# Optimization experiments

Measured on AMD Instinct MI355X. Metric: run time of the kernel, lower is better.

The kernel has to match this reference:

```python
import jax, jax.numpy as jnp
import numpy as np

N_EDGES, N_CH = 4, 2
N_NODES = 8192
IN_C, OUT_C = 64, 64


def setup_inputs() -> dict:
    key = jax.random.key(0)
    k1, k2, k3, k4, k5 = jax.random.split(key, 5)
    A = jax.random.uniform(k1, (N_EDGES, N_NODES, N_NODES), dtype=jnp.float32)
    X = jax.random.normal(k2, (N_NODES, IN_C), dtype=jnp.float32)
    weight = jax.random.normal(k3, (N_EDGES, N_CH), dtype=jnp.float32)
    # torch Linear: weight [out, in], bias [out]
    lin_w = jax.random.normal(k4, (OUT_C, IN_C), dtype=jnp.float32) / np.sqrt(IN_C)
    lin_b = jax.random.normal(k5, (OUT_C,), dtype=jnp.float32) * 0.01
    bias = jnp.zeros((OUT_C,), dtype=jnp.float32)
    return {"A": A, "X": X, "weight": weight, "lin_w": lin_w, "lin_b": lin_b, "bias": bias}


def reference(A, X, weight, lin_w, lin_b, bias):
    # softmax over edge dim (dim=0), then the double loop collapses to a
    # per-edge scale: A_agg = sum_i (sum_j fw[i,j]) * A[i]
    fw = jax.nn.softmax(weight, axis=0)          # [E, C]
    scale = fw.sum(axis=1)                        # [E]
    A_agg = jnp.einsum('e,enm->nm', scale, A)     # [N, N]
    H = A_agg @ X                                 # [N, in_c]
    H = H @ lin_w.T + lin_b + bias                # [N, out_c]
    return H
```

## Files before the change

### kernel.cpp

```cpp
#include <hip/hip_runtime.h>
#include <math.h>


#define NN 8192
#define CH 64
#define RB 16
#define KT 64
#define NT (NN / KT)
#define NBLK (NN / RB)

#define A_BUF_F 4096
#define OFF_A0 0
#define OFF_A1 (A_BUF_F)
#define OFF_X0 (2 * A_BUF_F)
#define AGG_STRIDE_S 72
#define AGG_F ((RB * AGG_STRIDE_S) / 2)
#define HT_STRIDE 68
#define XPACK_UINTS_PER_TILE 2048

typedef __attribute__((ext_vector_type(8))) short bf16x8;
typedef __attribute__((ext_vector_type(4))) float f32x4;

__device__ __forceinline__ void dma16(const float* g, float* l) {
  __builtin_amdgcn_global_load_lds(
      (const __attribute__((address_space(1))) void*)g,
      (__attribute__((address_space(3))) void*)l, 16, 0, 0);
}

__device__ __forceinline__ unsigned f2bfu(float f) {
  unsigned u = __float_as_uint(f);
  return (u + 0x7FFFu + ((u >> 16) & 1u)) >> 16;
}

__global__ __launch_bounds__(256)
void gtn_packX(const float* __restrict__ X, unsigned* __restrict__ ws) {
  const int F = blockIdx.x * 256 + threadIdx.x;
  const int t = F >> 9, rem = F & 511;
  const int wv = rem >> 7, kt = (rem >> 6) & 1, lane = rem & 63;
  const int fm = lane & 15, fg = lane >> 4;
  const int c = wv * 16 + fm;
  const int bk = t * KT + kt * 32 + fg * 8;
  uint4 o;
  o.x = f2bfu(X[(size_t)(bk + 0) * CH + c]) | (f2bfu(X[(size_t)(bk + 1) * CH + c]) << 16);
  o.y = f2bfu(X[(size_t)(bk + 2) * CH + c]) | (f2bfu(X[(size_t)(bk + 3) * CH + c]) << 16);
  o.z = f2bfu(X[(size_t)(bk + 4) * CH + c]) | (f2bfu(X[(size_t)(bk + 5) * CH + c]) << 16);
  o.w = f2bfu(X[(size_t)(bk + 6) * CH + c]) | (f2bfu(X[(size_t)(bk + 7) * CH + c]) << 16);
  *(uint4*)&ws[(size_t)F * 4] = o;
}

template<bool PACKED>
__global__ __launch_bounds__(256)
void gtn_fused(const float* __restrict__ A, const float* __restrict__ X,
               const unsigned* __restrict__ Xp,
               const float* __restrict__ Wt, const float* __restrict__ lw,
               const float* __restrict__ lb, const float* __restrict__ bias,
               float* __restrict__ out) {
  constexpr int XBUF_F   = PACKED ? 2048 : 4096;
  constexpr int OFF_X1   = OFF_X0 + XBUF_F;
  constexpr int OFF_AGG  = OFF_X0 + 2 * XBUF_F;
  constexpr int LDS_FLOATS = OFF_AGG + AGG_F;
  __shared__ __align__(16) float arena[LDS_FLOATS];

  const int tid = threadIdx.x;
  const int n0  = blockIdx.x * RB;

  float sc0, sc1, sc2, sc3;
  {
    float a0 = Wt[0], a1 = Wt[2], a2 = Wt[4], a3 = Wt[6];
    float b0 = Wt[1], b1 = Wt[3], b2 = Wt[5], b3 = Wt[7];
    float ma = fmaxf(fmaxf(a0, a1), fmaxf(a2, a3));
    float mb = fmaxf(fmaxf(b0, b1), fmaxf(b2, b3));
    float ea0 = expf(a0 - ma), ea1 = expf(a1 - ma), ea2 = expf(a2 - ma), ea3 = expf(a3 - ma);
    float eb0 = expf(b0 - mb), eb1 = expf(b1 - mb), eb2 = expf(b2 - mb), eb3 = expf(b3 - mb);
    float ra = 1.f / (ea0 + ea1 + ea2 + ea3);
    float rb = 1.f / (eb0 + eb1 + eb2 + eb3);
    sc0 = ea0 * ra + eb0 * rb;  sc1 = ea1 * ra + eb1 * rb;
    sc2 = ea2 * ra + eb2 * rb;  sc3 = ea3 * ra + eb3 * rb;
  }

  const float* gA[4];
#pragma unroll
  for (int i = 0; i < 4; ++i) {
    const int s = tid + i * 256;
    const int e = s >> 8, r = (s >> 4) & 15, kq = s & 15;
    gA[i] = A + ((size_t)e << 26) + (size_t)(n0 + r) * NN + kq * 4;
  }
  const float* gX[4];
  const unsigned* gXp[2];
  if (PACKED) {
#pragma unroll
    for (int i = 0; i < 2; ++i) gXp[i] = Xp + (size_t)(tid + i * 256) * 4;
  } else {
#pragma unroll
    for (int i = 0; i < 4; ++i) {
      const int s = tid + i * 256;
      const int kk = s >> 4, cq = s & 15;
      gX[i] = X + (size_t)kk * CH + cq * 4;
    }
  }

  const int rg = tid >> 4, cg = tid & 15;
  const int lane = tid & 63, wv = tid >> 6;
  const int ch0 = wv * 16;
  const int fm = lane & 15, fg = lane >> 4;

#pragma unroll
  for (int i = 0; i < 4; ++i) dma16(gA[i], &arena[OFF_A0 + (tid + i * 256) * 4]);
  if (PACKED) {
#pragma unroll
    for (int i = 0; i < 2; ++i)
      dma16((const float*)gXp[i], &arena[OFF_X0 + (tid + i * 256) * 4]);
  } else {
#pragma unroll
    for (int i = 0; i < 4; ++i) dma16(gX[i], &arena[OFF_X0 + (tid + i * 256) * 4]);
  }

  f32x4 acc = {0.f, 0.f, 0.f, 0.f};

  for (int t = 0; t < NT; ++t) {
    const int b = t & 1;

    asm volatile("s_waitcnt vmcnt(0)\n\ts_barrier" ::: "memory");

    if (t + 1 < NT) {
      float* Ad = &arena[b ? OFF_A0 : OFF_A1];
      float* Xd = &arena[b ? OFF_X0 : OFF_X1];
      const size_t koff = (size_t)(t + 1) * KT;
#pragma unroll
      for (int i = 0; i < 4; ++i) dma16(gA[i] + koff, Ad + (tid + i * 256) * 4);
      if (PACKED) {
        const size_t xoff = (size_t)(t + 1) * XPACK_UINTS_PER_TILE;
#pragma unroll
        for (int i = 0; i < 2; ++i)
          dma16((const float*)(gXp[i] + xoff), Xd + (tid + i * 256) * 4);
      } else {
#pragma unroll
        for (int i = 0; i < 4; ++i)
          dma16(gX[i] + koff * CH, Xd + (tid + i * 256) * 4);
      }
    }

    {
      const float* Ab = &arena[b ? OFF_A1 : OFF_A0];
      short* aggW = (short*)&arena[OFF_AGG];
      float gx = 0.f, gy = 0.f, gz = 0.f, gw = 0.f;
#pragma unroll
      for (int e = 0; e < 4; ++e) {
        const float s = (e == 0) ? sc0 : (e == 1) ? sc1 : (e == 2) ? sc2 : sc3;
        float4 v = *(const float4*)&Ab[(e * RB + rg) * KT + cg * 4];
        gx = fmaf(s, v.x, gx); gy = fmaf(s, v.y, gy);
        gz = fmaf(s, v.z, gz); gw = fmaf(s, v.w, gw);
      }
      unsigned u0 = f2bfu(gx) | (f2bfu(gy) << 16);
      unsigned u1 = f2bfu(gz) | (f2bfu(gw) << 16);
      *(uint2*)&aggW[rg * AGG_STRIDE_S + cg * 4] = make_uint2(u0, u1);
    }

    asm volatile("s_waitcnt lgkmcnt(0)\n\ts_barrier" ::: "memory");

    {
      const short* aggS = (const short*)&arena[OFF_AGG];
#pragma unroll
      for (int kt = 0; kt < 2; ++kt) {
        bf16x8 af = *(const bf16x8*)&aggS[fm * AGG_STRIDE_S + fg * 8 + kt * 32];
        if (PACKED) {
          const unsigned* XbU = (const unsigned*)&arena[b ? OFF_X1 : OFF_X0];
          union { uint4 q; bf16x8 v; } xu;
          xu.q = *(const uint4*)&XbU[(((wv << 1) | kt) * 64 + lane) * 4];
          acc = __builtin_amdgcn_mfma_f32_16x16x32_bf16(af, xu.v, acc, 0, 0, 0);
        } else {
          const float* Xb = &arena[b ? OFF_X1 : OFF_X0];
          union { bf16x8 v; unsigned u[4]; } bu;
#pragma unroll
          for (int p = 0; p < 4; ++p) {
            float x0 = Xb[(kt * 32 + fg * 8 + 2 * p    ) * CH + ch0 + fm];
            float x1 = Xb[(kt * 32 + fg * 8 + 2 * p + 1) * CH + ch0 + fm];
            bu.u[p] = f2bfu(x0) | (f2bfu(x1) << 16);
          }
          acc = __builtin_amdgcn_mfma_f32_16x16x32_bf16(af, bu.v, acc, 0, 0, 0);
        }
      }
    }
  }

  __syncthreads();
  float* hT = arena;
#pragma unroll
  for (int r = 0; r < 4; ++r)
    hT[(fg * 4 + r) * HT_STRIDE + ch0 + fm] = acc[r];
  __syncthreads();

  const int c0 = cg * 4;
  float s0 = lb[c0 + 0] + bias[c0 + 0];
  float s1 = lb[c0 + 1] + bias[c0 + 1];
  float s2 = lb[c0 + 2] + bias[c0 + 2];
  float s3 = lb[c0 + 3] + bias[c0 + 3];
#pragma unroll
  for (int k4 = 0; k4 < CH / 4; ++k4) {
    float4 hv = *(const float4*)&hT[rg * HT_STRIDE + k4 * 4];
    float4 w0 = *(const float4*)&lw[(size_t)(c0 + 0) * CH + k4 * 4];
    float4 w1 = *(const float4*)&lw[(size_t)(c0 + 1) * CH + k4 * 4];
    float4 w2 = *(const float4*)&lw[(size_t)(c0 + 2) * CH + k4 * 4];
    float4 w3 = *(const float4*)&lw[(size_t)(c0 + 3) * CH + k4 * 4];
    s0 += hv.x * w0.x + hv.y * w0.y + hv.z * w0.z + hv.w * w0.w;
    s1 += hv.x * w1.x + hv.y * w1.y + hv.z * w1.z + hv.w * w1.w;
    s2 += hv.x * w2.x + hv.y * w2.y + hv.z * w2.z + hv.w * w2.w;
    s3 += hv.x * w3.x + hv.y * w3.y + hv.z * w3.z + hv.w * w3.w;
  }
  *(float4*)&out[(size_t)(n0 + rg) * CH + c0] = make_float4(s0, s1, s2, s3);
}

extern "C" void kernel_launch(void* const* d_in, const int* in_sizes, int n_in,
                              void* d_out, int out_size, void* d_ws, size_t ws_size,
                              hipStream_t stream) {
  const float* A    = (const float*)d_in[0];
  const float* X    = (const float*)d_in[1];
  const float* Wt   = (const float*)d_in[2];
  const float* lw   = (const float*)d_in[3];
  const float* lb   = (const float*)d_in[4];
  const float* bias = (const float*)d_in[5];
  float* out = (float*)d_out;

  const size_t packBytes = (size_t)NT * XPACK_UINTS_PER_TILE * 4;
  if (ws_size >= packBytes) {
    gtn_packX<<<dim3(256), 256, 0, stream>>>(X, (unsigned*)d_ws);
    gtn_fused<true><<<dim3(NBLK), 256, 0, stream>>>(
        A, X, (const unsigned*)d_ws, Wt, lw, lb, bias, out);
  } else {
    gtn_fused<false><<<dim3(NBLK), 256, 0, stream>>>(
        A, X, nullptr, Wt, lw, lb, bias, out);
  }
}
```

Measured before the change: 199.8 us.

## Triple-buffer A/X tiles with partial vmcnt waits for deeper prefetch

Switches the LDS staging from double to triple buffering, so loads for tile t+2 are issued while tile t is combined and multiplied. It uses partial s_waitcnt vmcnt counts instead of draining every outstanding load each iteration, which keeps more global loads in flight to hide HBM latency in this bandwidth-bound stream over A. LDS use grows by one extra A and X buffer, which may reduce occupancy. The hand-counted vmcnt values are fragile if the compiler reorders or adds memory ops.

```diff
diff --git a/kernel.cpp b/kernel.cpp
--- a/kernel.cpp
+++ b/kernel.cpp
@@ -10,9 +10,6 @@
 #define NBLK (NN / RB)
 
 #define A_BUF_F 4096
-#define OFF_A0 0
-#define OFF_A1 (A_BUF_F)
-#define OFF_X0 (2 * A_BUF_F)
 #define AGG_STRIDE_S 72
 #define AGG_F ((RB * AGG_STRIDE_S) / 2)
 #define HT_STRIDE 68
@@ -55,9 +52,9 @@
                const float* __restrict__ Wt, const float* __restrict__ lw,
                const float* __restrict__ lb, const float* __restrict__ bias,
                float* __restrict__ out) {
-  constexpr int XBUF_F   = PACKED ? 2048 : 4096;
-  constexpr int OFF_X1   = OFF_X0 + XBUF_F;
-  constexpr int OFF_AGG  = OFF_X0 + 2 * XBUF_F;
+  constexpr int XBUF_F = PACKED ? 2048 : 4096;
+  constexpr int OFF_X  = 3 * A_BUF_F;
+  constexpr int OFF_AGG = OFF_X + 3 * XBUF_F;
   constexpr int LDS_FLOATS = OFF_AGG + AGG_F;
   __shared__ __align__(16) float arena[LDS_FLOATS];
 
@@ -85,9 +82,9 @@
     const int e = s >> 8, r = (s >> 4) & 15, kq = s & 15;
     gA[i] = A + ((size_t)e << 26) + (size_t)(n0 + r) * NN + kq * 4;
   }
+  const unsigned* gXp[2];
   const float* gX[4];
-  const unsigned* gXp[2];
-  if (PACKED) {
+  if constexpr (PACKED) {
 #pragma unroll
     for (int i = 0; i < 2; ++i) gXp[i] = Xp + (size_t)(tid + i * 256) * 4;
   } else {
@@ -104,83 +101,110 @@
   const int ch0 = wv * 16;
   const int fm = lane & 15, fg = lane >> 4;
 
-#pragma unroll
-  for (int i = 0; i < 4; ++i) dma16(gA[i], &arena[OFF_A0 + (tid + i * 256) * 4]);
-  if (PACKED) {
-#pragma unroll
-    for (int i = 0; i < 2; ++i)
-      dma16((const float*)gXp[i], &arena[OFF_X0 + (tid + i * 256) * 4]);
-  } else {
-#pragma unroll
-    for (int i = 0; i < 4; ++i) dma16(gX[i], &arena[OFF_X0 + (tid + i * 256) * 4]);
-  }
+  auto issueS = [&](int u, int bi) {
+    const size_t koff = (size_t)u * KT;
+    float* Ad = &arena[bi * A_BUF_F];
+    float* Xd = &arena[OFF_X + bi * XBUF_F];
+#pragma unroll
+    for (int i = 0; i < 4; ++i) dma16(gA[i] + koff, Ad + (tid + i * 256) * 4);
+    if constexpr (PACKED) {
+      const size_t xoff = (size_t)u * XPACK_UINTS_PER_TILE;
+#pragma unroll
+      for (int i = 0; i < 2; ++i)
+        dma16((const float*)(gXp[i] + xoff), Xd + (tid + i * 256) * 4);
+    } else {
+#pragma unroll
+      for (int i = 0; i < 4; ++i)
+        dma16(gX[i] + koff * CH, Xd + (tid + i * 256) * 4);
+    }
+  };
+
+  auto combine = [&](int bi) {
+    const float* Ab = &arena[bi * A_BUF_F];
+    short* aggW = (short*)&arena[OFF_AGG];
+    float gx = 0.f, gy = 0.f, gz = 0.f, gw = 0.f;
+#pragma unroll
+    for (int e = 0; e < 4; ++e) {
+      const float s = (e == 0) ? sc0 : (e == 1) ? sc1 : (e == 2) ? sc2 : sc3;
+      float4 v = *(const float4*)&Ab[(e * RB + rg) * KT + cg * 4];
+      gx = fmaf(s, v.x, gx); gy = fmaf(s, v.y, gy);
+      gz = fmaf(s, v.z, gz); gw = fmaf(s, v.w, gw);
+    }
+    unsigned u0 = f2bfu(gx) | (f2bfu(gy) << 16);
+    unsigned u1 = f2bfu(gz) | (f2bfu(gw) << 16);
+    *(uint2*)&aggW[rg * AGG_STRIDE_S + cg * 4] = make_uint2(u0, u1);
+  };
 
   f32x4 acc = {0.f, 0.f, 0.f, 0.f};
 
-  for (int t = 0; t < NT; ++t) {
-    const int b = t & 1;
-
-    asm volatile("s_waitcnt vmcnt(0)\n\ts_barrier" ::: "memory");
-
-    if (t + 1 < NT) {
-      float* Ad = &arena[b ? OFF_A0 : OFF_A1];
-      float* Xd = &arena[b ? OFF_X0 : OFF_X1];
-      const size_t koff = (size_t)(t + 1) * KT;
-#pragma unroll
-      for (int i = 0; i < 4; ++i) dma16(gA[i] + koff, Ad + (tid + i * 256) * 4);
-      if (PACKED) {
-        const size_t xoff = (size_t)(t + 1) * XPACK_UINTS_PER_TILE;
-#pragma unroll
-        for (int i = 0; i < 2; ++i)
-          dma16((const float*)(gXp[i] + xoff), Xd + (tid + i * 256) * 4);
+  auto domfma = [&](int bi) {
+    const short* aggS = (const short*)&arena[OFF_AGG];
+#pragma unroll
+    for (int kt = 0; kt < 2; ++kt) {
+      bf16x8 af = *(const bf16x8*)&aggS[fm * AGG_STRIDE_S + fg * 8 + kt * 32];
+      if constexpr (PACKED) {
+        const unsigned* XbU = (const unsigned*)&arena[OFF_X + bi * XBUF_F];
+        union { uint4 q; bf16x8 v; } xu;
+        xu.q = *(const uint4*)&XbU[(((wv << 1) | kt) * 64 + lane) * 4];
+        acc = __builtin_amdgcn_mfma_f32_16x16x32_bf16(af, xu.v, acc, 0, 0, 0);
       } else {
-#pragma unroll
-        for (int i = 0; i < 4; ++i)
-          dma16(gX[i] + koff * CH, Xd + (tid + i * 256) * 4);
+        const float* Xb = &arena[OFF_X + bi * XBUF_F];
+        union { bf16x8 v; unsigned u[4]; } bu;
+#pragma unroll
+        for (int p = 0; p < 4; ++p) {
+          float x0 = Xb[(kt * 32 + fg * 8 + 2 * p    ) * CH + ch0 + fm];
+          float x1 = Xb[(kt * 32 + fg * 8 + 2 * p + 1) * CH + ch0 + fm];
+          bu.u[p] = f2bfu(x0) | (f2bfu(x1) << 16);
+        }
+        acc = __builtin_amdgcn_mfma_f32_16x16x32_bf16(af, bu.v, acc, 0, 0, 0);
       }
     }
-
-    {
-      const float* Ab = &arena[b ? OFF_A1 : OFF_A0];
-      short* aggW = (short*)&arena[OFF_AGG];
-      float gx = 0.f, gy = 0.f, gz = 0.f, gw = 0.f;
-#pragma unroll
-      for (int e = 0; e < 4; ++e) {
-        const float s = (e == 0) ? sc0 : (e == 1) ? sc1 : (e == 2) ? sc2 : sc3;
-        float4 v = *(const float4*)&Ab[(e * RB + rg) * KT + cg * 4];
-        gx = fmaf(s, v.x, gx); gy = fmaf(s, v.y, gy);
-        gz = fmaf(s, v.z, gz); gw = fmaf(s, v.w, gw);
-      }
-      unsigned u0 = f2bfu(gx) | (f2bfu(gy) << 16);
-      unsigned u1 = f2bfu(gz) | (f2bfu(gw) << 16);
-      *(uint2*)&aggW[rg * AGG_STRIDE_S + cg * 4] = make_uint2(u0, u1);
-    }
-
+  };
+
+  issueS(0, 0);
+  issueS(1, 1);
+
+  int bi = 0;
+  for (int t = 0; t < NT - 2; ++t) {
+    int b2 = bi + 2; if (b2 >= 3) b2 -= 3;
+    if constexpr (PACKED)
+      asm volatile("s_waitcnt vmcnt(8)\n\ts_barrier" ::: "memory");
+    else
+      asm volatile("s_waitcnt vmcnt(12)\n\ts_barrier" ::: "memory");
+    issueS(t + 2, b2);
+    combine(bi);
     asm volatile("s_waitcnt lgkmcnt(0)\n\ts_barrier" ::: "memory");
-
-    {
-      const short* aggS = (const short*)&arena[OFF_AGG];
-#pragma unroll
-      for (int kt = 0; kt < 2; ++kt) {
-        bf16x8 af = *(const bf16x8*)&aggS[fm * AGG_STRIDE_S + fg * 8 + kt * 32];
-        if (PACKED) {
-          const unsigned* XbU = (const unsigned*)&arena[b ? OFF_X1 : OFF_X0];
-          union { uint4 q; bf16x8 v; } xu;
-          xu.q = *(const uint4*)&XbU[(((wv << 1) | kt) * 64 + lane) * 4];
-          acc = __builtin_amdgcn_mfma_f32_16x16x32_bf16(af, xu.v, acc, 0, 0, 0);
-        } else {
-          const float* Xb = &arena[b ? OFF_X1 : OFF_X0];
-          union { bf16x8 v; unsigned u[4]; } bu;
-#pragma unroll
-          for (int p = 0; p < 4; ++p) {
-            float x0 = Xb[(kt * 32 + fg * 8 + 2 * p    ) * CH + ch0 + fm];
-            float x1 = Xb[(kt * 32 + fg * 8 + 2 * p + 1) * CH + ch0 + fm];
-            bu.u[p] = f2bfu(x0) | (f2bfu(x1) << 16);
-          }
-          acc = __builtin_amdgcn_mfma_f32_16x16x32_bf16(af, bu.v, acc, 0, 0, 0);
-        }
-      }
-    }
+    if constexpr (PACKED)
+      asm volatile("s_waitcnt vmcnt(12)" ::: "memory");
+    else
+      asm volatile("s_waitcnt vmcnt(16)" ::: "memory");
+    domfma(bi);
+    ++bi; if (bi == 3) bi = 0;
+  }
+
+  {
+    if constexpr (PACKED)
+      asm volatile("s_waitcnt vmcnt(8)\n\ts_barrier" ::: "memory");
+    else
+      asm volatile("s_waitcnt vmcnt(12)\n\ts_barrier" ::: "memory");
+    combine(bi);
+    asm volatile("s_waitcnt lgkmcnt(0)\n\ts_barrier" ::: "memory");
+    if constexpr (PACKED)
+      asm volatile("s_waitcnt vmcnt(6)" ::: "memory");
+    else
+      asm volatile("s_waitcnt vmcnt(8)" ::: "memory");
+    domfma(bi);
+    ++bi; if (bi == 3) bi = 0;
+  }
+  {
+    if constexpr (PACKED)
+      asm volatile("s_waitcnt vmcnt(2)\n\ts_barrier" ::: "memory");
+    else
+      asm volatile("s_waitcnt vmcnt(4)\n\ts_barrier" ::: "memory");
+    combine(bi);
+    asm volatile("s_waitcnt lgkmcnt(0)\n\ts_barrier" ::: "memory");
+    asm volatile("s_waitcnt vmcnt(0)" ::: "memory");
+    domfma(bi);
   }
 
   __syncthreads();
```

After: 198.0 us. Within noise of the previous version (-0.9%).
